# Kernel tuning notes

Hardware: AMD Instinct MI355X
Metric: run time of the kernel (lower is better)

## Reference

```python
import jax, jax.numpy as jnp
import numpy as np

B, S, D = 4, 2048, 1024
H = 16
HD = D // H

def setup_inputs() -> dict:
    key = jax.random.key(0)
    ks = jax.random.split(key, 6)
    scale = 1.0 / np.sqrt(D)
    x = jax.random.normal(ks[0], (B, S, D), dtype=jnp.float32)
    Wq = jax.random.normal(ks[1], (D, D), dtype=jnp.float32) * scale
    Wk = jax.random.normal(ks[2], (D, D), dtype=jnp.float32) * scale
    Wv = jax.random.normal(ks[3], (D, D), dtype=jnp.float32) * scale
    Wo = jax.random.normal(ks[4], (D, D), dtype=jnp.float32) * scale
    bo = jax.random.normal(ks[5], (D,), dtype=jnp.float32) * 0.01
    return {"x": x, "Wq": Wq, "Wk": Wk, "Wv": Wv, "Wo": Wo, "bo": bo}

def reference(x, Wq, Wk, Wv, Wo, bo):
    b, n, _ = x.shape
    # QKV projections (no bias), split into heads: [b, h, n, hd]
    q = (x @ Wq).reshape(b, n, H, HD).transpose(0, 2, 1, 3)
    k = (x @ Wk).reshape(b, n, H, HD).transpose(0, 2, 1, 3)
    v = (x @ Wv).reshape(b, n, H, HD).transpose(0, 2, 1, 3)
    scores = jnp.einsum('bhqd,bhkd->bhqk', q, k) / jnp.sqrt(jnp.float32(HD))
    causal = jnp.tril(jnp.ones((n, n), dtype=bool))
    scores = jnp.where(causal, scores, -jnp.inf)
    attn = jax.nn.softmax(scores, axis=-1)  # dropout p=0.0 -> identity
    ctx = jnp.einsum('bhqk,bhkd->bhqd', attn, v)
    ctx = ctx.transpose(0, 2, 1, 3).reshape(b, n, D)
    return ctx @ Wo + bo
```

## Files before the change

kernel.cpp:

```cpp
#include <hip/hip_runtime.h>

#define S_   2048
#define D_   1024
#define H_   16
#define HD_  64
#define NTOK 8192
#define QKS  2048
#define QSCALE 0.18033688f

typedef __attribute__((ext_vector_type(8))) __bf16 bf16x8;
typedef __attribute__((ext_vector_type(4))) __bf16 bf16x4;
typedef __attribute__((ext_vector_type(4))) float  f32x4;
typedef __attribute__((ext_vector_type(4))) short  short4v;

#define GPTR(p) ((__attribute__((address_space(1))) void*)(unsigned long long)(p))
#define LPTR(p) ((__attribute__((address_space(3))) void*)(p))

__global__ __launch_bounds__(256) void k_prep(const float* __restrict__ x,
                                              __bf16* __restrict__ xb,
                                              const float* __restrict__ Wq,
                                              const float* __restrict__ Wk,
                                              const float* __restrict__ Wv,
                                              const float* __restrict__ Wo,
                                              __bf16* __restrict__ wqkt,
                                              __bf16* __restrict__ wvt,
                                              __bf16* __restrict__ wot) {
    const int bx = blockIdx.x;
    if (bx < 4096) {
        int i = bx * 2048 + threadIdx.x * 8;
        f32x4 a = *(const f32x4*)(x + i);
        f32x4 b = *(const f32x4*)(x + i + 4);
        bf16x8 o;
#pragma unroll
        for (int j = 0; j < 4; j++) { o[j] = (__bf16)a[j]; o[4 + j] = (__bf16)b[j]; }
        *(bf16x8*)(xb + i) = o;
        return;
    }
    __shared__ float t[32][33];
    const int tt = bx - 4096;
    const int widx = tt >> 10, r = tt & 1023;
    const float* W;
    __bf16* Wt;
    switch (widx) {
        case 0: W = Wq; Wt = wqkt; break;
        case 1: W = Wk; Wt = wqkt + (size_t)D_ * D_; break;
        case 2: W = Wv; Wt = wvt; break;
        default: W = Wo; Wt = wot; break;
    }
    const int i0 = (r & 31) * 32, j0 = (r >> 5) * 32;
    const int tx = threadIdx.x & 31, ty = threadIdx.x >> 5;
#pragma unroll
    for (int rr = 0; rr < 32; rr += 8)
        t[ty + rr][tx] = W[(size_t)(i0 + ty + rr) * D_ + j0 + tx];
    __syncthreads();
#pragma unroll
    for (int rr = 0; rr < 32; rr += 8)
        Wt[(size_t)(j0 + ty + rr) * D_ + i0 + tx] = (__bf16)t[tx][ty + rr];
}

__device__ __forceinline__ void gemm_body_bf16(const __bf16* __restrict__ A,
                                               const __bf16* __restrict__ Bt,
                                               __bf16* __restrict__ C,
                                               int N, int K, int tm, int tn,
                                               float scale, int vperm,
                                               __bf16* As, __bf16* Bs) {
    const int tid  = threadIdx.x;
    const int wave = tid >> 6, lane = tid & 63;
    const int quad = lane >> 4, l16 = lane & 15;
    const int wm = (wave & 1) * 64, wn = (wave >> 1) * 64;
    f32x4 acc[4][4] = {};

    for (int k0 = 0; k0 < K; k0 += 32) {
        __syncthreads();
#pragma unroll
        for (int s = 0; s < 2; s++) {
            const int cb = s * 256 + wave * 64;
            const int c  = cb + lane;
            const int row = c >> 2;
            const int kc  = ((c & 3) ^ ((row >> 1) & 3)) * 8;
            __builtin_amdgcn_global_load_lds(GPTR(A + (size_t)(tm + row) * K + k0 + kc),
                                             LPTR(As + cb * 8), 16, 0, 0);
            __builtin_amdgcn_global_load_lds(GPTR(Bt + (size_t)(tn + row) * K + k0 + kc),
                                             LPTR(Bs + cb * 8), 16, 0, 0);
        }
        __syncthreads();

        bf16x8 af[4], bf[4];
#pragma unroll
        for (int mi = 0; mi < 4; mi++) {
            const int rf = wm + mi * 16 + l16;
            af[mi] = *(const bf16x8*)&As[rf * 32 + (quad ^ ((rf >> 1) & 3)) * 8];
        }
#pragma unroll
        for (int ni = 0; ni < 4; ni++) {
            const int rf = wn + ni * 16 + l16;
            bf[ni] = *(const bf16x8*)&Bs[rf * 32 + (quad ^ ((rf >> 1) & 3)) * 8];
        }
#pragma unroll
        for (int mi = 0; mi < 4; mi++)
#pragma unroll
            for (int ni = 0; ni < 4; ni++)
                acc[mi][ni] = __builtin_amdgcn_mfma_f32_16x16x32_bf16(
                    af[mi], bf[ni], acc[mi][ni], 0, 0, 0);
    }

#pragma unroll
    for (int mi = 0; mi < 4; mi++)
#pragma unroll
        for (int ni = 0; ni < 4; ni++)
#pragma unroll
            for (int r = 0; r < 4; r++) {
                const int row = tm + wm + mi * 16 + quad * 4 + r;
                const int col = tn + wn + ni * 16 + l16;
                const int xr  = (vperm & (row >> 3) & 1) << 2;
                C[(size_t)row * N + (col ^ xr)] = (__bf16)(acc[mi][ni][r] * scale);
            }
}

__global__ __launch_bounds__(256) void k_gemm_qkv(const __bf16* __restrict__ xb,
                                                  const __bf16* __restrict__ wqkt,
                                                  const __bf16* __restrict__ wvt,
                                                  __bf16* __restrict__ qk,
                                                  __bf16* __restrict__ VT) {
    __shared__ __bf16 As[128 * 32];
    __shared__ __bf16 Bs[128 * 32];
    const int bx = blockIdx.x;
    if (bx < 1024) {
        const int tm = (bx & 63) * 128, tn = (bx >> 6) * 128;
        const float scale = (tn < D_) ? QSCALE : 1.0f;
        gemm_body_bf16(xb, wqkt, qk, QKS, D_, tm, tn, scale, 0, As, Bs);
    } else {
        const int b2 = bx - 1024;
        const int tn = (b2 & 63) * 128, tm = (b2 >> 6) * 128;
        gemm_body_bf16(wvt, xb, VT, NTOK, D_, tm, tn, 1.0f, 1, As, Bs);
    }
}

__global__ __launch_bounds__(256) void k_gemm_o(const __bf16* __restrict__ A,
                                                const __bf16* __restrict__ Bt,
                                                float* __restrict__ C,
                                                const float* __restrict__ bias) {
    __shared__ __bf16 As[128 * 32];
    __shared__ __bf16 Bs[128 * 32];
    const int tid  = threadIdx.x;
    const int wave = tid >> 6, lane = tid & 63;
    const int quad = lane >> 4, l16 = lane & 15;
    const int tm = blockIdx.x * 128, tn = blockIdx.y * 128;
    const int wm = (wave & 1) * 64, wn = (wave >> 1) * 64;
    const int N = D_, K = D_;
    f32x4 acc[4][4] = {};

    for (int k0 = 0; k0 < K; k0 += 32) {
        __syncthreads();
#pragma unroll
        for (int s = 0; s < 2; s++) {
            const int cb = s * 256 + wave * 64;
            const int c  = cb + lane;
            const int row = c >> 2;
            const int kc  = ((c & 3) ^ ((row >> 1) & 3)) * 8;
            __builtin_amdgcn_global_load_lds(GPTR(A + (size_t)(tm + row) * K + k0 + kc),
                                             LPTR(As + cb * 8), 16, 0, 0);
            __builtin_amdgcn_global_load_lds(GPTR(Bt + (size_t)(tn + row) * K + k0 + kc),
                                             LPTR(Bs + cb * 8), 16, 0, 0);
        }
        __syncthreads();

        bf16x8 af[4], bf[4];
#pragma unroll
        for (int mi = 0; mi < 4; mi++) {
            const int rf = wm + mi * 16 + l16;
            af[mi] = *(const bf16x8*)&As[rf * 32 + (quad ^ ((rf >> 1) & 3)) * 8];
        }
#pragma unroll
        for (int ni = 0; ni < 4; ni++) {
            const int rf = wn + ni * 16 + l16;
            bf[ni] = *(const bf16x8*)&Bs[rf * 32 + (quad ^ ((rf >> 1) & 3)) * 8];
        }
#pragma unroll
        for (int mi = 0; mi < 4; mi++)
#pragma unroll
            for (int ni = 0; ni < 4; ni++)
                acc[mi][ni] = __builtin_amdgcn_mfma_f32_16x16x32_bf16(
                    af[mi], bf[ni], acc[mi][ni], 0, 0, 0);
    }

#pragma unroll
    for (int mi = 0; mi < 4; mi++)
#pragma unroll
        for (int ni = 0; ni < 4; ni++)
#pragma unroll
            for (int r = 0; r < 4; r++) {
                const int row = tm + wm + mi * 16 + quad * 4 + r;
                const int col = tn + wn + ni * 16 + l16;
                C[(size_t)row * N + col] = acc[mi][ni][r] + bias[col];
            }
}

__device__ __forceinline__ short bf16_bits(float f) {
    __bf16 h = (__bf16)f;
    return __builtin_bit_cast(short, h);
}

__global__ __launch_bounds__(256, 2) void k_attn(const __bf16* __restrict__ Qb,
                                                 const __bf16* __restrict__ Kb,
                                                 const __bf16* __restrict__ VT,
                                                 __bf16* __restrict__ ctx) {
    __shared__ __bf16 Ks[2][64 * 64];
    __shared__ __bf16 Vs[2][64 * 64];

    const int tid = threadIdx.x;
    const int wave = tid >> 6, lane = tid & 63;
    const int quad = lane >> 4, l16 = lane & 15;
    const int bid = blockIdx.x;
    const int hb  = ((bid >> 6) << 3) | (bid & 7);
    const int qp  = (bid >> 3) & 7;
    const int h = hb >> 2, b = hb & 3;
    const size_t tok0 = (size_t)b * S_;
    const size_t hoff = (size_t)h * HD_;

    auto stage = [&](int kv, int buf) {
#pragma unroll
        for (int s = 0; s < 2; s++) {
            const int cb = s * 256 + wave * 64;
            const int c  = cb + lane;
            const int row = c >> 3;
            const int gc  = (c & 7) ^ (row & 7);
            __builtin_amdgcn_global_load_lds(
                GPTR(Kb + (size_t)(tok0 + kv + row) * QKS + hoff + gc * 8),
                LPTR(&Ks[buf][cb * 8]), 16, 0, 0);
            __builtin_amdgcn_global_load_lds(
                GPTR(VT + (hoff + row) * (size_t)NTOK + tok0 + kv + gc * 8),
                LPTR(&Vs[buf][cb * 8]), 16, 0, 0);
        }
    };

#pragma unroll 1
    for (int sidx = 0; sidx < 2; sidx++) {
        const int qt = sidx == 0 ? qp : 15 - qp;
        const int qb = qt * 128;
        const int q0 = qb + wave * 32;

        bf16x8 qf[2][2];
#pragma unroll
        for (int qi = 0; qi < 2; qi++)
#pragma unroll
            for (int ks = 0; ks < 2; ks++)
                qf[qi][ks] = *(const bf16x8*)&Qb[(tok0 + q0 + qi * 16 + l16) * QKS +
                                                 hoff + ks * 32 + quad * 8];

        f32x4 oacc[2][4] = {};
        float lsum[2] = {0.f, 0.f};
        const int ktb = (qb + 127) >> 6;

        stage(0, 0);
        __syncthreads();

        for (int kt = 0; kt <= ktb; kt++) {
            const int cur = kt & 1;
            const int kv0 = kt * 64;
            if (kt < ktb) stage(kv0 + 64, 1 - cur);

            if (kv0 <= q0 + 31) {
                f32x4 st[2][4] = {};
#pragma unroll
                for (int ks = 0; ks < 2; ks++)
#pragma unroll
                    for (int ksub = 0; ksub < 4; ksub++) {
                        const int r = ksub * 16 + l16;
                        bf16x8 kf = *(const bf16x8*)
                            &Ks[cur][(r * 8 + (((ks * 4 + quad) ^ (r & 7)))) * 8];
#pragma unroll
                        for (int qi = 0; qi < 2; qi++)
                            st[qi][ksub] = __builtin_amdgcn_mfma_f32_16x16x32_bf16(
                                kf, qf[qi][ks], st[qi][ksub], 0, 0, 0);
                    }
                if (kv0 + 63 > q0) {
#pragma unroll
                    for (int qi = 0; qi < 2; qi++)
#pragma unroll
                        for (int ksub = 0; ksub < 4; ksub++)
#pragma unroll
                            for (int r = 0; r < 4; r++) {
                                const int kg = kv0 + ksub * 16 + quad * 4 + r;
                                const int qg = q0 + qi * 16 + l16;
                                if (kg > qg) st[qi][ksub][r] = -1e30f;
                            }
                }
                short4v pfrag[2][4];
#pragma unroll
                for (int qi = 0; qi < 2; qi++)
#pragma unroll
                    for (int ksub = 0; ksub < 4; ksub++) {
                        float p0 = __builtin_amdgcn_exp2f(st[qi][ksub][0]);
                        float p1 = __builtin_amdgcn_exp2f(st[qi][ksub][1]);
                        float p2 = __builtin_amdgcn_exp2f(st[qi][ksub][2]);
                        float p3 = __builtin_amdgcn_exp2f(st[qi][ksub][3]);
                        lsum[qi] += (p0 + p1) + (p2 + p3);
                        short4v pf = {bf16_bits(p0), bf16_bits(p1),
                                      bf16_bits(p2), bf16_bits(p3)};
                        pfrag[qi][ksub] = pf;
                    }
#pragma unroll
                for (int ksub = 0; ksub < 4; ksub++)
#pragma unroll
                    for (int hs = 0; hs < 4; hs++) {
                        const int row = hs * 16 + l16;
                        const int swz = (ksub * 2 + (quad >> 1)) ^ (row & 7);
                        short4v vf = *(const short4v*)
                            &Vs[cur][row * 64 + swz * 8 + ((quad ^ (l16 >> 3)) & 1) * 4];
#pragma unroll
                        for (int qi = 0; qi < 2; qi++)
                            oacc[qi][hs] = __builtin_amdgcn_mfma_f32_16x16x16bf16_1k(
                                vf, pfrag[qi][ksub], oacc[qi][hs], 0, 0, 0);
                    }
            }
            __syncthreads();
        }

#pragma unroll
        for (int qi = 0; qi < 2; qi++) {
            float v = lsum[qi];
            v += __shfl_xor(v, 16);
            v += __shfl_xor(v, 32);
            const float rl = 1.0f / v;
#pragma unroll
            for (int hs = 0; hs < 4; hs++) {
                bf16x4 o;
#pragma unroll
                for (int r = 0; r < 4; r++) o[r] = (__bf16)(oacc[qi][hs][r] * rl);
                *(bf16x4*)&ctx[(tok0 + q0 + qi * 16 + l16) * D_ + hoff +
                               hs * 16 + quad * 4] = o;
            }
        }
    }
}

extern "C" void kernel_launch(void* const* d_in, const int* in_sizes, int n_in,
                              void* d_out, int out_size, void* d_ws, size_t ws_size,
                              hipStream_t stream) {
    const float* x  = (const float*)d_in[0];
    const float* Wq = (const float*)d_in[1];
    const float* Wk = (const float*)d_in[2];
    const float* Wv = (const float*)d_in[3];
    const float* Wo = (const float*)d_in[4];
    const float* bo = (const float*)d_in[5];
    float* out = (float*)d_out;

    char* p = (char*)d_ws;
    __bf16* xb   = (__bf16*)p; p += (size_t)NTOK * D_ * 2;
    __bf16* wqkt = (__bf16*)p; p += (size_t)2 * D_ * D_ * 2;
    __bf16* wvt  = (__bf16*)p; p += (size_t)D_ * D_ * 2;
    __bf16* wot  = (__bf16*)p; p += (size_t)D_ * D_ * 2;
    __bf16* qk   = (__bf16*)p; p += (size_t)NTOK * QKS * 2;
    __bf16* VT   = (__bf16*)p; p += (size_t)NTOK * D_ * 2;
    __bf16* ctx  = (__bf16*)p; p += (size_t)NTOK * D_ * 2;

    k_prep<<<dim3(4096 + 4 * 1024), 256, 0, stream>>>(x, xb, Wq, Wk, Wv, Wo,
                                                      wqkt, wvt, wot);
    k_gemm_qkv<<<dim3(1024 + 512), 256, 0, stream>>>(xb, wqkt, wvt, qk, VT);
    k_attn<<<dim3(512), 256, 0, stream>>>(qk, qk + D_, VT, ctx);
    k_gemm_o<<<dim3(64, 8), 256, 0, stream>>>(ctx, wot, out, bo);
}
```

Measured before the change: 232.1 us.

## Double-buffer LDS tiles in QKV and output projection GEMMs

```diff
diff --git a/kernel.cpp b/kernel.cpp
--- a/kernel.cpp
+++ b/kernel.cpp
@@ -70,8 +70,7 @@
     const int wm = (wave & 1) * 64, wn = (wave >> 1) * 64;
     f32x4 acc[4][4] = {};
 
-    for (int k0 = 0; k0 < K; k0 += 32) {
-        __syncthreads();
+    auto stage = [&](int k0, int buf) {
 #pragma unroll
         for (int s = 0; s < 2; s++) {
             const int cb = s * 256 + wave * 64;
@@ -79,22 +78,31 @@
             const int row = c >> 2;
             const int kc  = ((c & 3) ^ ((row >> 1) & 3)) * 8;
             __builtin_amdgcn_global_load_lds(GPTR(A + (size_t)(tm + row) * K + k0 + kc),
-                                             LPTR(As + cb * 8), 16, 0, 0);
+                                             LPTR(As + buf * 4096 + cb * 8), 16, 0, 0);
             __builtin_amdgcn_global_load_lds(GPTR(Bt + (size_t)(tn + row) * K + k0 + kc),
-                                             LPTR(Bs + cb * 8), 16, 0, 0);
-        }
-        __syncthreads();
-
+                                             LPTR(Bs + buf * 4096 + cb * 8), 16, 0, 0);
+        }
+    };
+
+    stage(0, 0);
+    __syncthreads();
+
+    int cur = 0;
+    for (int k0 = 0; k0 < K; k0 += 32) {
+        if (k0 + 32 < K) stage(k0 + 32, cur ^ 1);
+
+        const __bf16* Asb = As + cur * 4096;
+        const __bf16* Bsb = Bs + cur * 4096;
         bf16x8 af[4], bf[4];
 #pragma unroll
         for (int mi = 0; mi < 4; mi++) {
             const int rf = wm + mi * 16 + l16;
-            af[mi] = *(const bf16x8*)&As[rf * 32 + (quad ^ ((rf >> 1) & 3)) * 8];
+            af[mi] = *(const bf16x8*)&Asb[rf * 32 + (quad ^ ((rf >> 1) & 3)) * 8];
         }
 #pragma unroll
         for (int ni = 0; ni < 4; ni++) {
             const int rf = wn + ni * 16 + l16;
-            bf[ni] = *(const bf16x8*)&Bs[rf * 32 + (quad ^ ((rf >> 1) & 3)) * 8];
+            bf[ni] = *(const bf16x8*)&Bsb[rf * 32 + (quad ^ ((rf >> 1) & 3)) * 8];
         }
 #pragma unroll
         for (int mi = 0; mi < 4; mi++)
@@ -102,6 +110,9 @@
             for (int ni = 0; ni < 4; ni++)
                 acc[mi][ni] = __builtin_amdgcn_mfma_f32_16x16x32_bf16(
                     af[mi], bf[ni], acc[mi][ni], 0, 0, 0);
+
+        __syncthreads();
+        cur ^= 1;
     }
 
 #pragma unroll
@@ -117,13 +128,13 @@
             }
 }
 
-__global__ __launch_bounds__(256) void k_gemm_qkv(const __bf16* __restrict__ xb,
-                                                  const __bf16* __restrict__ wqkt,
-                                                  const __bf16* __restrict__ wvt,
-                                                  __bf16* __restrict__ qk,
-                                                  __bf16* __restrict__ VT) {
-    __shared__ __bf16 As[128 * 32];
-    __shared__ __bf16 Bs[128 * 32];
+__global__ __launch_bounds__(256, 4) void k_gemm_qkv(const __bf16* __restrict__ xb,
+                                                     const __bf16* __restrict__ wqkt,
+                                                     const __bf16* __restrict__ wvt,
+                                                     __bf16* __restrict__ qk,
+                                                     __bf16* __restrict__ VT) {
+    __shared__ __bf16 As[2 * 128 * 32];
+    __shared__ __bf16 Bs[2 * 128 * 32];
     const int bx = blockIdx.x;
     if (bx < 1024) {
         const int tm = (bx & 63) * 128, tn = (bx >> 6) * 128;
@@ -136,12 +147,12 @@
     }
 }
 
-__global__ __launch_bounds__(256) void k_gemm_o(const __bf16* __restrict__ A,
-                                                const __bf16* __restrict__ Bt,
-                                                float* __restrict__ C,
-                                                const float* __restrict__ bias) {
-    __shared__ __bf16 As[128 * 32];
-    __shared__ __bf16 Bs[128 * 32];
+__global__ __launch_bounds__(256, 4) void k_gemm_o(const __bf16* __restrict__ A,
+                                                   const __bf16* __restrict__ Bt,
+                                                   float* __restrict__ C,
+                                                   const float* __restrict__ bias) {
+    __shared__ __bf16 As[2 * 128 * 32];
+    __shared__ __bf16 Bs[2 * 128 * 32];
     const int tid  = threadIdx.x;
     const int wave = tid >> 6, lane = tid & 63;
     const int quad = lane >> 4, l16 = lane & 15;
@@ -150,8 +161,7 @@
     const int N = D_, K = D_;
     f32x4 acc[4][4] = {};
 
-    for (int k0 = 0; k0 < K; k0 += 32) {
-        __syncthreads();
+    auto stage = [&](int k0, int buf) {
 #pragma unroll
         for (int s = 0; s < 2; s++) {
             const int cb = s * 256 + wave * 64;
@@ -159,22 +169,31 @@
             const int row = c >> 2;
             const int kc  = ((c & 3) ^ ((row >> 1) & 3)) * 8;
             __builtin_amdgcn_global_load_lds(GPTR(A + (size_t)(tm + row) * K + k0 + kc),
-                                             LPTR(As + cb * 8), 16, 0, 0);
+                                             LPTR(As + buf * 4096 + cb * 8), 16, 0, 0);
             __builtin_amdgcn_global_load_lds(GPTR(Bt + (size_t)(tn + row) * K + k0 + kc),
-                                             LPTR(Bs + cb * 8), 16, 0, 0);
-        }
-        __syncthreads();
-
+                                             LPTR(Bs + buf * 4096 + cb * 8), 16, 0, 0);
+        }
+    };
+
+    stage(0, 0);
+    __syncthreads();
+
+    int cur = 0;
+    for (int k0 = 0; k0 < K; k0 += 32) {
+        if (k0 + 32 < K) stage(k0 + 32, cur ^ 1);
+
+        const __bf16* Asb = As + cur * 4096;
+        const __bf16* Bsb = Bs + cur * 4096;
         bf16x8 af[4], bf[4];
 #pragma unroll
         for (int mi = 0; mi < 4; mi++) {
             const int rf = wm + mi * 16 + l16;
-            af[mi] = *(const bf16x8*)&As[rf * 32 + (quad ^ ((rf >> 1) & 3)) * 8];
+            af[mi] = *(const bf16x8*)&Asb[rf * 32 + (quad ^ ((rf >> 1) & 3)) * 8];
         }
 #pragma unroll
         for (int ni = 0; ni < 4; ni++) {
             const int rf = wn + ni * 16 + l16;
-            bf[ni] = *(const bf16x8*)&Bs[rf * 32 + (quad ^ ((rf >> 1) & 3)) * 8];
+            bf[ni] = *(const bf16x8*)&Bsb[rf * 32 + (quad ^ ((rf >> 1) & 3)) * 8];
         }
 #pragma unroll
         for (int mi = 0; mi < 4; mi++)
@@ -182,6 +201,9 @@
             for (int ni = 0; ni < 4; ni++)
                 acc[mi][ni] = __builtin_amdgcn_mfma_f32_16x16x32_bf16(
                     af[mi], bf[ni], acc[mi][ni], 0, 0, 0);
+
+        __syncthreads();
+        cur ^= 1;
     }
 
 #pragma unroll
```

After: 235.5 us. No clear change (+1.5%).

## Rewrite QKV GEMM as 256x256 tile, double-buffered, phased pipeline with 512 threads

Applied to the files above, without the earlier changes.

```diff
diff --git a/kernel.cpp b/kernel.cpp
--- a/kernel.cpp
+++ b/kernel.cpp
@@ -58,81 +58,135 @@
         Wt[(size_t)(j0 + ty + rr) * D_ + i0 + tx] = (__bf16)t[tx][ty + rr];
 }
 
-__device__ __forceinline__ void gemm_body_bf16(const __bf16* __restrict__ A,
-                                               const __bf16* __restrict__ Bt,
-                                               __bf16* __restrict__ C,
-                                               int N, int K, int tm, int tn,
-                                               float scale, int vperm,
-                                               __bf16* As, __bf16* Bs) {
-    const int tid  = threadIdx.x;
+#define VMW(n) asm volatile("s_waitcnt vmcnt(" #n ")" ::: "memory")
+
+#define PHASE(QM, QN, STAGE_STMT, WAIT_STMT) do {                                  \
+    bf16x8 af[4][2], bfr[2][2];                                                    \
+    _Pragma("unroll")                                                              \
+    for (int mi = 0; mi < 4; mi++) {                                               \
+        const int row = wr * 128 + (QM) * 64 + mi * 16 + l16;                      \
+        _Pragma("unroll")                                                          \
+        for (int ks = 0; ks < 2; ks++)                                             \
+            af[mi][ks] = *(const bf16x8*)&Ac[row * 64 +                            \
+                                             ((ks * 4 + quad) ^ (row & 7)) * 8];   \
+    }                                                                              \
+    _Pragma("unroll")                                                              \
+    for (int ni = 0; ni < 2; ni++) {                                               \
+        const int rho = wc * 32 + ni * 16 + l16;                                   \
+        _Pragma("unroll")                                                          \
+        for (int ks = 0; ks < 2; ks++)                                             \
+            bfr[ni][ks] = *(const bf16x8*)&Bc[((QN) * 128 + rho) * 64 +            \
+                                              ((ks * 4 + quad) ^ (rho & 7)) * 8];  \
+    }                                                                              \
+    STAGE_STMT;                                                                    \
+    __builtin_amdgcn_s_barrier();                                                  \
+    asm volatile("s_waitcnt lgkmcnt(0)" ::: "memory");                             \
+    __builtin_amdgcn_sched_barrier(0);                                             \
+    __builtin_amdgcn_s_setprio(1);                                                 \
+    _Pragma("unroll")                                                              \
+    for (int mi = 0; mi < 4; mi++)                                                 \
+        _Pragma("unroll")                                                          \
+        for (int ni = 0; ni < 2; ni++)                                             \
+            _Pragma("unroll")                                                      \
+            for (int ks = 0; ks < 2; ks++)                                         \
+                acc[(QM) * 4 + mi][(QN) * 2 + ni] =                                \
+                    __builtin_amdgcn_mfma_f32_16x16x32_bf16(                       \
+                        af[mi][ks], bfr[ni][ks],                                   \
+                        acc[(QM) * 4 + mi][(QN) * 2 + ni], 0, 0, 0);               \
+    __builtin_amdgcn_s_setprio(0);                                                 \
+    WAIT_STMT;                                                                     \
+    __builtin_amdgcn_s_barrier();                                                  \
+    __builtin_amdgcn_sched_barrier(0);                                             \
+} while (0)
+
+__device__ __forceinline__ void gemm256_body(const __bf16* __restrict__ Ag,
+                                             const __bf16* __restrict__ Bg,
+                                             __bf16* __restrict__ C,
+                                             int N, int K, int tm, int tn,
+                                             float scale, int vperm,
+                                             __bf16* As0, __bf16* Bs0) {
+    const int tid = threadIdx.x;
     const int wave = tid >> 6, lane = tid & 63;
     const int quad = lane >> 4, l16 = lane & 15;
-    const int wm = (wave & 1) * 64, wn = (wave >> 1) * 64;
-    f32x4 acc[4][4] = {};
-
-    for (int k0 = 0; k0 < K; k0 += 32) {
-        __syncthreads();
+    const int wr = wave >> 2, wc = wave & 3;
+    f32x4 acc[8][4] = {};
+
+    auto stageA = [&](int kt, int pair) {
+        __bf16* dst = As0 + (kt & 1) * 16384;
+        const int k0 = kt * 64;
+#pragma unroll
+        for (int uu = 0; uu < 2; uu++) {
+            const int u = pair + uu * 2;
+            const int r = u * 64 + (tid >> 3);
+            const int c = (tid & 7) ^ (r & 7);
+            __builtin_amdgcn_global_load_lds(
+                GPTR(Ag + (size_t)(tm + r) * K + k0 + c * 8),
+                LPTR(dst + u * 4096 + wave * 512), 16, 0, 0);
+        }
+    };
+    auto stageB = [&](int kt, int g) {
+        __bf16* dst = Bs0 + (kt & 1) * 16384 + g * 8192;
+        const int k0 = kt * 64;
 #pragma unroll
         for (int s = 0; s < 2; s++) {
-            const int cb = s * 256 + wave * 64;
-            const int c  = cb + lane;
-            const int row = c >> 2;
-            const int kc  = ((c & 3) ^ ((row >> 1) & 3)) * 8;
-            __builtin_amdgcn_global_load_lds(GPTR(A + (size_t)(tm + row) * K + k0 + kc),
-                                             LPTR(As + cb * 8), 16, 0, 0);
-            __builtin_amdgcn_global_load_lds(GPTR(Bt + (size_t)(tn + row) * K + k0 + kc),
-                                             LPTR(Bs + cb * 8), 16, 0, 0);
-        }
-        __syncthreads();
-
-        bf16x8 af[4], bf[4];
-#pragma unroll
-        for (int mi = 0; mi < 4; mi++) {
-            const int rf = wm + mi * 16 + l16;
-            af[mi] = *(const bf16x8*)&As[rf * 32 + (quad ^ ((rf >> 1) & 3)) * 8];
-        }
-#pragma unroll
-        for (int ni = 0; ni < 4; ni++) {
-            const int rf = wn + ni * 16 + l16;
-            bf[ni] = *(const bf16x8*)&Bs[rf * 32 + (quad ^ ((rf >> 1) & 3)) * 8];
-        }
-#pragma unroll
-        for (int mi = 0; mi < 4; mi++)
-#pragma unroll
-            for (int ni = 0; ni < 4; ni++)
-                acc[mi][ni] = __builtin_amdgcn_mfma_f32_16x16x32_bf16(
-                    af[mi], bf[ni], acc[mi][ni], 0, 0, 0);
-    }
-
-#pragma unroll
-    for (int mi = 0; mi < 4; mi++)
+            const int rho = s * 64 + (tid >> 3);
+            const int br  = (rho >> 5) * 64 + g * 32 + (rho & 31);
+            const int c   = (tid & 7) ^ (rho & 7);
+            __builtin_amdgcn_global_load_lds(
+                GPTR(Bg + (size_t)(tn + br) * K + k0 + c * 8),
+                LPTR(dst + s * 4096 + wave * 512), 16, 0, 0);
+        }
+    };
+
+    stageA(0, 0); stageB(0, 0); stageA(0, 1); stageB(0, 1);
+    VMW(4);
+    __builtin_amdgcn_s_barrier();
+    __builtin_amdgcn_sched_barrier(0);
+
+    const int T = K >> 6;
+    for (int kt = 0; kt < T; kt++) {
+        const __bf16* Ac = As0 + (kt & 1) * 16384;
+        const __bf16* Bc = Bs0 + (kt & 1) * 16384;
+        const bool pre = (kt + 1 < T);
+        PHASE(0, 0, { if (pre) stageA(kt + 1, 0); },
+                    { if (pre) { VMW(4); } else { VMW(2); } });
+        PHASE(1, 0, { if (pre) stageB(kt + 1, 0); },
+                    { if (pre) { VMW(4); } else { VMW(0); } });
+        PHASE(0, 1, { if (pre) stageA(kt + 1, 1); }, {});
+        PHASE(1, 1, { if (pre) stageB(kt + 1, 1); },
+                    { if (pre) { VMW(4); } });
+    }
+
+#pragma unroll
+    for (int mi = 0; mi < 8; mi++)
 #pragma unroll
         for (int ni = 0; ni < 4; ni++)
 #pragma unroll
             for (int r = 0; r < 4; r++) {
-                const int row = tm + wm + mi * 16 + quad * 4 + r;
-                const int col = tn + wn + ni * 16 + l16;
+                const int row = tm + wr * 128 + (mi >> 2) * 64 + (mi & 3) * 16 +
+                                quad * 4 + r;
+                const int col = tn + wc * 64 + (ni >> 1) * 32 + (ni & 1) * 16 + l16;
                 const int xr  = (vperm & (row >> 3) & 1) << 2;
                 C[(size_t)row * N + (col ^ xr)] = (__bf16)(acc[mi][ni][r] * scale);
             }
 }
 
-__global__ __launch_bounds__(256) void k_gemm_qkv(const __bf16* __restrict__ xb,
-                                                  const __bf16* __restrict__ wqkt,
-                                                  const __bf16* __restrict__ wvt,
-                                                  __bf16* __restrict__ qk,
-                                                  __bf16* __restrict__ VT) {
-    __shared__ __bf16 As[128 * 32];
-    __shared__ __bf16 Bs[128 * 32];
+__global__ __launch_bounds__(512, 2) void k_gemm_qkv(const __bf16* __restrict__ xb,
+                                                     const __bf16* __restrict__ wqkt,
+                                                     const __bf16* __restrict__ wvt,
+                                                     __bf16* __restrict__ qk,
+                                                     __bf16* __restrict__ VT) {
+    __shared__ __bf16 As[2 * 16384];
+    __shared__ __bf16 Bs[2 * 16384];
     const int bx = blockIdx.x;
-    if (bx < 1024) {
-        const int tm = (bx & 63) * 128, tn = (bx >> 6) * 128;
+    if (bx < 256) {
+        const int tm = (bx & 31) * 256, tn = (bx >> 5) * 256;
         const float scale = (tn < D_) ? QSCALE : 1.0f;
-        gemm_body_bf16(xb, wqkt, qk, QKS, D_, tm, tn, scale, 0, As, Bs);
+        gemm256_body(xb, wqkt, qk, QKS, D_, tm, tn, scale, 0, As, Bs);
     } else {
-        const int b2 = bx - 1024;
-        const int tn = (b2 & 63) * 128, tm = (b2 >> 6) * 128;
-        gemm_body_bf16(wvt, xb, VT, NTOK, D_, tm, tn, 1.0f, 1, As, Bs);
+        const int b2 = bx - 256;
+        const int tn = (b2 & 31) * 256, tm = (b2 >> 5) * 256;
+        gemm256_body(wvt, xb, VT, NTOK, D_, tm, tn, 1.0f, 1, As, Bs);
     }
 }
 
@@ -357,7 +411,7 @@
 
     k_prep<<<dim3(4096 + 4 * 1024), 256, 0, stream>>>(x, xb, Wq, Wk, Wv, Wo,
                                                       wqkt, wvt, wot);
-    k_gemm_qkv<<<dim3(1024 + 512), 256, 0, stream>>>(xb, wqkt, wvt, qk, VT);
+    k_gemm_qkv<<<dim3(256 + 128), 512, 0, stream>>>(xb, wqkt, wvt, qk, VT);
     k_attn<<<dim3(512), 256, 0, stream>>>(qk, qk + D_, VT, ctx);
     k_gemm_o<<<dim3(64, 8), 256, 0, stream>>>(ctx, wot, out, bo);
 }
```

New measurement: 258.1 us. +11.2%, slower.

## Double-buffer GEMM k-loop with 256x128 tiles, 512 threads, 64-wide K steps

Applied to the files above, without the earlier changes.

```diff
diff --git a/kernel.cpp b/kernel.cpp
--- a/kernel.cpp
+++ b/kernel.cpp
@@ -58,50 +58,72 @@
         Wt[(size_t)(j0 + ty + rr) * D_ + i0 + tx] = (__bf16)t[tx][ty + rr];
 }
 
-__device__ __forceinline__ void gemm_body_bf16(const __bf16* __restrict__ A,
-                                               const __bf16* __restrict__ Bt,
-                                               __bf16* __restrict__ C,
-                                               int N, int K, int tm, int tn,
-                                               float scale, int vperm,
-                                               __bf16* As, __bf16* Bs) {
+__device__ __forceinline__ void gemm_body_256x128(const __bf16* __restrict__ A,
+                                                  const __bf16* __restrict__ Bt,
+                                                  __bf16* __restrict__ C,
+                                                  int N, int K, int tm, int tn,
+                                                  float scale, int vperm,
+                                                  __bf16* As, __bf16* Bs) {
     const int tid  = threadIdx.x;
     const int wave = tid >> 6, lane = tid & 63;
     const int quad = lane >> 4, l16 = lane & 15;
-    const int wm = (wave & 1) * 64, wn = (wave >> 1) * 64;
+    const int wrow = (wave >> 1) * 64, wcol = (wave & 1) * 64;
+    const int lr = lane >> 3, lc = lane & 7;
     f32x4 acc[4][4] = {};
 
-    for (int k0 = 0; k0 < K; k0 += 32) {
+    auto stage = [&](int kt) {
+        const int k0 = kt * 64;
+        __bf16* Ad = As + (kt & 1) * 16384;
+        __bf16* Bd = Bs + (kt & 1) * 8192;
+        const int cs = (lc ^ lr) * 8;
+#pragma unroll
+        for (int u = 0; u < 4; u++) {
+            const int r = u * 64 + wave * 8 + lr;
+            __builtin_amdgcn_global_load_lds(GPTR(A + (size_t)(tm + r) * K + k0 + cs),
+                                             LPTR(Ad + (u * 64 + wave * 8) * 64), 16, 0, 0);
+        }
+#pragma unroll
+        for (int u = 0; u < 2; u++) {
+            const int r = u * 64 + wave * 8 + lr;
+            __builtin_amdgcn_global_load_lds(GPTR(Bt + (size_t)(tn + r) * K + k0 + cs),
+                                             LPTR(Bd + (u * 64 + wave * 8) * 64), 16, 0, 0);
+        }
+    };
+
+    stage(0);
+    __syncthreads();
+
+    const int T = K >> 6;
+    for (int kt = 0; kt < T; kt++) {
+        if (kt + 1 < T) stage(kt + 1);
+
+        const __bf16* Ac = As + (kt & 1) * 16384;
+        const __bf16* Bc = Bs + (kt & 1) * 8192;
+        bf16x8 af[4][2], bf[4][2];
+#pragma unroll
+        for (int mi = 0; mi < 4; mi++) {
+            const int row = wrow + mi * 16 + l16;
+#pragma unroll
+            for (int ks = 0; ks < 2; ks++)
+                af[mi][ks] = *(const bf16x8*)&Ac[row * 64 + ((ks * 4 + quad) ^ (row & 7)) * 8];
+        }
+#pragma unroll
+        for (int ni = 0; ni < 4; ni++) {
+            const int row = wcol + ni * 16 + l16;
+#pragma unroll
+            for (int ks = 0; ks < 2; ks++)
+                bf[ni][ks] = *(const bf16x8*)&Bc[row * 64 + ((ks * 4 + quad) ^ (row & 7)) * 8];
+        }
+#pragma unroll
+        for (int ks = 0; ks < 2; ks++)
+#pragma unroll
+            for (int mi = 0; mi < 4; mi++)
+#pragma unroll
+                for (int ni = 0; ni < 4; ni++)
+                    acc[mi][ni] = __builtin_amdgcn_mfma_f32_16x16x32_bf16(
+                        af[mi][ks], bf[ni][ks], acc[mi][ni], 0, 0, 0);
+
         __syncthreads();
-#pragma unroll
-        for (int s = 0; s < 2; s++) {
-            const int cb = s * 256 + wave * 64;
-            const int c  = cb + lane;
-            const int row = c >> 2;
-            const int kc  = ((c & 3) ^ ((row >> 1) & 3)) * 8;
-            __builtin_amdgcn_global_load_lds(GPTR(A + (size_t)(tm + row) * K + k0 + kc),
-                                             LPTR(As + cb * 8), 16, 0, 0);
-            __builtin_amdgcn_global_load_lds(GPTR(Bt + (size_t)(tn + row) * K + k0 + kc),
-                                             LPTR(Bs + cb * 8), 16, 0, 0);
-        }
-        __syncthreads();
-
-        bf16x8 af[4], bf[4];
-#pragma unroll
-        for (int mi = 0; mi < 4; mi++) {
-            const int rf = wm + mi * 16 + l16;
-            af[mi] = *(const bf16x8*)&As[rf * 32 + (quad ^ ((rf >> 1) & 3)) * 8];
-        }
-#pragma unroll
-        for (int ni = 0; ni < 4; ni++) {
-            const int rf = wn + ni * 16 + l16;
-            bf[ni] = *(const bf16x8*)&Bs[rf * 32 + (quad ^ ((rf >> 1) & 3)) * 8];
-        }
-#pragma unroll
-        for (int mi = 0; mi < 4; mi++)
-#pragma unroll
-            for (int ni = 0; ni < 4; ni++)
-                acc[mi][ni] = __builtin_amdgcn_mfma_f32_16x16x32_bf16(
-                    af[mi], bf[ni], acc[mi][ni], 0, 0, 0);
     }
 
 #pragma unroll
@@ -110,78 +132,100 @@
         for (int ni = 0; ni < 4; ni++)
 #pragma unroll
             for (int r = 0; r < 4; r++) {
-                const int row = tm + wm + mi * 16 + quad * 4 + r;
-                const int col = tn + wn + ni * 16 + l16;
+                const int row = tm + wrow + mi * 16 + quad * 4 + r;
+                const int col = tn + wcol + ni * 16 + l16;
                 const int xr  = (vperm & (row >> 3) & 1) << 2;
                 C[(size_t)row * N + (col ^ xr)] = (__bf16)(acc[mi][ni][r] * scale);
             }
 }
 
-__global__ __launch_bounds__(256) void k_gemm_qkv(const __bf16* __restrict__ xb,
-                                                  const __bf16* __restrict__ wqkt,
-                                                  const __bf16* __restrict__ wvt,
-                                                  __bf16* __restrict__ qk,
-                                                  __bf16* __restrict__ VT) {
-    __shared__ __bf16 As[128 * 32];
-    __shared__ __bf16 Bs[128 * 32];
+__global__ __launch_bounds__(512, 2) void k_gemm_qkv(const __bf16* __restrict__ xb,
+                                                     const __bf16* __restrict__ wqkt,
+                                                     const __bf16* __restrict__ wvt,
+                                                     __bf16* __restrict__ qk,
+                                                     __bf16* __restrict__ VT) {
+    __shared__ __bf16 As[2 * 16384];
+    __shared__ __bf16 Bs[2 * 8192];
     const int bx = blockIdx.x;
-    if (bx < 1024) {
-        const int tm = (bx & 63) * 128, tn = (bx >> 6) * 128;
+    if (bx < 512) {
+        const int tm = (bx & 31) * 256, tn = (bx >> 5) * 128;
         const float scale = (tn < D_) ? QSCALE : 1.0f;
-        gemm_body_bf16(xb, wqkt, qk, QKS, D_, tm, tn, scale, 0, As, Bs);
+        gemm_body_256x128(xb, wqkt, qk, QKS, D_, tm, tn, scale, 0, As, Bs);
     } else {
-        const int b2 = bx - 1024;
-        const int tn = (b2 & 63) * 128, tm = (b2 >> 6) * 128;
-        gemm_body_bf16(wvt, xb, VT, NTOK, D_, tm, tn, 1.0f, 1, As, Bs);
-    }
-}
-
-__global__ __launch_bounds__(256) void k_gemm_o(const __bf16* __restrict__ A,
-                                                const __bf16* __restrict__ Bt,
-                                                float* __restrict__ C,
-                                                const float* __restrict__ bias) {
-    __shared__ __bf16 As[128 * 32];
-    __shared__ __bf16 Bs[128 * 32];
+        const int b2 = bx - 512;
+        const int tn = (b2 & 63) * 128, tm = (b2 >> 6) * 256;
+        gemm_body_256x128(wvt, xb, VT, NTOK, D_, tm, tn, 1.0f, 1, As, Bs);
+    }
+}
+
+__global__ __launch_bounds__(512, 2) void k_gemm_o(const __bf16* __restrict__ A,
+                                                   const __bf16* __restrict__ Bt,
+                                                   float* __restrict__ C,
+                                                   const float* __restrict__ bias) {
+    __shared__ __bf16 As[2 * 16384];
+    __shared__ __bf16 Bs[2 * 8192];
     const int tid  = threadIdx.x;
     const int wave = tid >> 6, lane = tid & 63;
     const int quad = lane >> 4, l16 = lane & 15;
-    const int tm = blockIdx.x * 128, tn = blockIdx.y * 128;
-    const int wm = (wave & 1) * 64, wn = (wave >> 1) * 64;
+    const int wrow = (wave >> 1) * 64, wcol = (wave & 1) * 64;
+    const int lr = lane >> 3, lc = lane & 7;
+    const int tm = (blockIdx.x & 31) * 256, tn = (blockIdx.x >> 5) * 128;
     const int N = D_, K = D_;
     f32x4 acc[4][4] = {};
 
-    for (int k0 = 0; k0 < K; k0 += 32) {
+    auto stage = [&](int kt) {
+        const int k0 = kt * 64;
+        __bf16* Ad = As + (kt & 1) * 16384;
+        __bf16* Bd = Bs + (kt & 1) * 8192;
+        const int cs = (lc ^ lr) * 8;
+#pragma unroll
+        for (int u = 0; u < 4; u++) {
+            const int r = u * 64 + wave * 8 + lr;
+            __builtin_amdgcn_global_load_lds(GPTR(A + (size_t)(tm + r) * K + k0 + cs),
+                                             LPTR(Ad + (u * 64 + wave * 8) * 64), 16, 0, 0);
+        }
+#pragma unroll
+        for (int u = 0; u < 2; u++) {
+            const int r = u * 64 + wave * 8 + lr;
+            __builtin_amdgcn_global_load_lds(GPTR(Bt + (size_t)(tn + r) * K + k0 + cs),
+                                             LPTR(Bd + (u * 64 + wave * 8) * 64), 16, 0, 0);
+        }
+    };
+
+    stage(0);
+    __syncthreads();
+
+    const int T = K >> 6;
+    for (int kt = 0; kt < T; kt++) {
+        if (kt + 1 < T) stage(kt + 1);
+
+        const __bf16* Ac = As + (kt & 1) * 16384;
+        const __bf16* Bc = Bs + (kt & 1) * 8192;
+        bf16x8 af[4][2], bf[4][2];
+#pragma unroll
+        for (int mi = 0; mi < 4; mi++) {
+            const int row = wrow + mi * 16 + l16;
+#pragma unroll
+            for (int ks = 0; ks < 2; ks++)
+                af[mi][ks] = *(const bf16x8*)&Ac[row * 64 + ((ks * 4 + quad) ^ (row & 7)) * 8];
+        }
+#pragma unroll
+        for (int ni = 0; ni < 4; ni++) {
+            const int row = wcol + ni * 16 + l16;
+#pragma unroll
+            for (int ks = 0; ks < 2; ks++)
+                bf[ni][ks] = *(const bf16x8*)&Bc[row * 64 + ((ks * 4 + quad) ^ (row & 7)) * 8];
+        }
+#pragma unroll
+        for (int ks = 0; ks < 2; ks++)
+#pragma unroll
+            for (int mi = 0; mi < 4; mi++)
+#pragma unroll
+                for (int ni = 0; ni < 4; ni++)
+                    acc[mi][ni] = __builtin_amdgcn_mfma_f32_16x16x32_bf16(
+                        af[mi][ks], bf[ni][ks], acc[mi][ni], 0, 0, 0);
+
         __syncthreads();
-#pragma unroll
-        for (int s = 0; s < 2; s++) {
-            const int cb = s * 256 + wave * 64;
-            const int c  = cb + lane;
-            const int row = c >> 2;
-            const int kc  = ((c & 3) ^ ((row >> 1) & 3)) * 8;
-            __builtin_amdgcn_global_load_lds(GPTR(A + (size_t)(tm + row) * K + k0 + kc),
-                                             LPTR(As + cb * 8), 16, 0, 0);
-            __builtin_amdgcn_global_load_lds(GPTR(Bt + (size_t)(tn + row) * K + k0 + kc),
-                                             LPTR(Bs + cb * 8), 16, 0, 0);
-        }
-        __syncthreads();
-
-        bf16x8 af[4], bf[4];
-#pragma unroll
-        for (int mi = 0; mi < 4; mi++) {
-            const int rf = wm + mi * 16 + l16;
-            af[mi] = *(const bf16x8*)&As[rf * 32 + (quad ^ ((rf >> 1) & 3)) * 8];
-        }
-#pragma unroll
-        for (int ni = 0; ni < 4; ni++) {
-            const int rf = wn + ni * 16 + l16;
-            bf[ni] = *(const bf16x8*)&Bs[rf * 32 + (quad ^ ((rf >> 1) & 3)) * 8];
-        }
-#pragma unroll
-        for (int mi = 0; mi < 4; mi++)
-#pragma unroll
-            for (int ni = 0; ni < 4; ni++)
-                acc[mi][ni] = __builtin_amdgcn_mfma_f32_16x16x32_bf16(
-                    af[mi], bf[ni], acc[mi][ni], 0, 0, 0);
     }
 
 #pragma unroll
@@ -190,8 +234,8 @@
         for (int ni = 0; ni < 4; ni++)
 #pragma unroll
             for (int r = 0; r < 4; r++) {
-                const int row = tm + wm + mi * 16 + quad * 4 + r;
-                const int col = tn + wn + ni * 16 + l16;
+                const int row = tm + wrow + mi * 16 + quad * 4 + r;
+                const int col = tn + wcol + ni * 16 + l16;
                 C[(size_t)row * N + col] = acc[mi][ni][r] + bias[col];
             }
 }
@@ -357,7 +401,7 @@
 
     k_prep<<<dim3(4096 + 4 * 1024), 256, 0, stream>>>(x, xb, Wq, Wk, Wv, Wo,
                                                       wqkt, wvt, wot);
-    k_gemm_qkv<<<dim3(1024 + 512), 256, 0, stream>>>(xb, wqkt, wvt, qk, VT);
+    k_gemm_qkv<<<dim3(512 + 256), 512, 0, stream>>>(xb, wqkt, wvt, qk, VT);
     k_attn<<<dim3(512), 256, 0, stream>>>(qk, qk + D_, VT, ctx);
-    k_gemm_o<<<dim3(64, 8), 256, 0, stream>>>(ctx, wot, out, bo);
-}
+    k_gemm_o<<<dim3(256), 512, 0, stream>>>(ctx, wot, out, bo);
+}
```

Measured after the change: 254.3 us. +9.6%, slower.
